# Optimization experiments

Measured on AMD Instinct MI355X. Metric: run time of the kernel, lower is better.

Reference implementation:

```python
import jax, jax.numpy as jnp
import numpy as np

EMB_DIM = 256
N_EMBED = 1024
BETA = 0.25


def setup_inputs() -> dict:
    key = jax.random.key(0)
    k1, k2 = jax.random.split(key)
    encoderout = jax.random.normal(k1, (32, EMB_DIM, 32, 32), dtype=jnp.float32)
    # embedding.weight.data.normal_(mean=0, std=1/n_embed)
    codebook = jax.random.normal(k2, (N_EMBED, EMB_DIM), dtype=jnp.float32) * (1.0 / N_EMBED)
    return {"encoderout": encoderout, "codebook": codebook}


def reference(encoderout, codebook):
    # NCHW -> NHWC
    x = jnp.transpose(encoderout, (0, 2, 3, 1))  # [B,H,W,D]
    flat = x.reshape(-1, EMB_DIM)                # [N,D]
    d2 = (jnp.sum(flat * flat, axis=1, keepdims=True)
          + jnp.sum(codebook * codebook, axis=1)[None, :]
          - 2.0 * flat @ codebook.T)             # [N,K]
    idx = jnp.argmin(d2, axis=1)                 # [N]
    quant = codebook[idx].reshape(x.shape)       # [B,H,W,D]
    codebook_loss = jnp.mean((quant - jax.lax.stop_gradient(x)) ** 2)
    commitment_loss = jnp.mean((x - jax.lax.stop_gradient(quant)) ** 2)
    loss = codebook_loss + BETA * commitment_loss
    # FAITHFUL to source bug: straight-through output is overwritten by the
    # input permuted back to NCHW, so out == encoderout.
    out = jnp.transpose(x, (0, 3, 1, 2))
    return (out, loss, codebook_loss, commitment_loss)
```

## Files before the change

### kernel.cpp

```cpp
#include <hip/hip_runtime.h>
#include <stdint.h>


#define EMB 256
#define ELEMS 8388608

typedef __bf16 bf16x8 __attribute__((ext_vector_type(8)));
typedef float  f32x4  __attribute__((ext_vector_type(4)));

union Frag { uint4 u4; bf16x8 v; };

__device__ __forceinline__ unsigned short f2bf(float f) {
    unsigned u = __float_as_uint(f);
    u += 0x7FFFu + ((u >> 16) & 1u);
    return (unsigned short)(u >> 16);
}

__global__ __launch_bounds__(256) void vq_prep(const float* __restrict__ cb,
                                               uint2* __restrict__ cbswz,
                                               float* __restrict__ esq) {
    const int tid  = threadIdx.x;
    const int w    = tid >> 6;
    const int lane = tid & 63;
    const int n    = blockIdx.x * 4 + w;

    const float4* row = (const float4*)(cb + n * EMB);
    float4 v = row[lane];

    float s = v.x * v.x + v.y * v.y + v.z * v.z + v.w * v.w;
    #pragma unroll
    for (int m = 1; m <= 32; m <<= 1) s += __shfl_xor(s, m);
    if (lane == 0) esq[n] = s;

    unsigned lo = (unsigned)f2bf(v.x) | ((unsigned)f2bf(v.y) << 16);
    unsigned hi = (unsigned)f2bf(v.z) | ((unsigned)f2bf(v.w) << 16);
    int kc = lane >> 1;
    int h  = lane & 1;
    cbswz[n * 64 + ((kc ^ (n & 7)) << 1) + h] = make_uint2(lo, hi);
}

__global__ __launch_bounds__(512, 2) void vq_main(const float* __restrict__ enc,
                                                  const uint4* __restrict__ cbswz,
                                                  const float* __restrict__ esq,
                                                  float* __restrict__ out,
                                                  float* __restrict__ accum) {
    __shared__ uint4 As[2048];
    __shared__ uint4 Bs[2048];
    __shared__ float dmin[4][64];
    __shared__ float partsA[8];

    const int tid  = threadIdx.x;
    const int w    = tid >> 6;
    const int lane = tid & 63;
    const int q    = lane >> 4;
    const int c    = lane & 15;
    const int wm   = w >> 2;
    const int wn   = w & 3;

    const int b   = blockIdx.x >> 4;
    const int hw0 = (blockIdx.x & 15) << 6;
    const float* encB = enc + (size_t)b * 262144 + hw0;
    float*       outB = out + (size_t)b * 262144 + hw0;

    const int q4 = tid & 15;
    const int kg = tid >> 4;
    union { float4 f4; float f[4]; } v[8];
    #pragma unroll
    for (int j = 0; j < 8; ++j)
        v[j].f4 = *(const float4*)(encB + (size_t)(kg * 8 + j) * 1024 + q4 * 4);

    float sx = 0.f;
    #pragma unroll
    for (int j = 0; j < 8; ++j) {
        *(float4*)(outB + (size_t)(kg * 8 + j) * 1024 + q4 * 4) = v[j].f4;
        sx = fmaf(v[j].f[0], v[j].f[0], sx);
        sx = fmaf(v[j].f[1], v[j].f[1], sx);
        sx = fmaf(v[j].f[2], v[j].f[2], sx);
        sx = fmaf(v[j].f[3], v[j].f[3], sx);
    }
    #pragma unroll
    for (int i = 0; i < 4; ++i) {
        unsigned short us[8];
        #pragma unroll
        for (int j = 0; j < 8; ++j) us[j] = f2bf(v[j].f[i]);
        uint4 pk;
        pk.x = (unsigned)us[0] | ((unsigned)us[1] << 16);
        pk.y = (unsigned)us[2] | ((unsigned)us[3] << 16);
        pk.z = (unsigned)us[4] | ((unsigned)us[5] << 16);
        pk.w = (unsigned)us[6] | ((unsigned)us[7] << 16);
        const int r = q4 * 4 + i;
        As[r * 32 + (kg ^ (r & 7))] = pk;
    }
    #pragma unroll
    for (int m = 1; m <= 32; m <<= 1) sx += __shfl_xor(sx, m);
    if (lane == 0) partsA[w] = sx;
    __syncthreads();

    bf16x8 afr[2][8];
    #pragma unroll
    for (int mi = 0; mi < 2; ++mi) {
        const int r = wm * 32 + mi * 16 + c;
        #pragma unroll
        for (int ks = 0; ks < 8; ++ks) {
            Frag fa; fa.u4 = As[r * 32 + ((ks * 4 + q) ^ (r & 7))];
            afr[mi][ks] = fa.v;
        }
    }

    float rmin[2][4];
    #pragma unroll
    for (int mi = 0; mi < 2; ++mi)
        #pragma unroll
        for (int r2 = 0; r2 < 4; ++r2) rmin[mi][r2] = 1e30f;

    const char* cbbase = (const char*)cbswz;
    const int nl = wn * 16 + c;

    for (int nc = 0; nc < 16; ++nc) {
        __syncthreads();
        #pragma unroll
        for (int i = 0; i < 4; ++i) {
            const int o = (i * 8 + w) * 1024;
            __builtin_amdgcn_global_load_lds(
                (const __attribute__((address_space(1))) unsigned int*)
                    (cbbase + nc * 32768 + o + lane * 16),
                (__attribute__((address_space(3))) unsigned int*)((char*)Bs + o),
                16, 0, 0);
        }
        __syncthreads();

        f32x4 acc0 = (f32x4){0.f, 0.f, 0.f, 0.f};
        f32x4 acc1 = (f32x4){0.f, 0.f, 0.f, 0.f};
        #pragma unroll
        for (int ks = 0; ks < 8; ++ks) {
            Frag fb; fb.u4 = Bs[nl * 32 + ((ks * 4 + q) ^ (nl & 7))];
            acc0 = __builtin_amdgcn_mfma_f32_16x16x32_bf16(afr[0][ks], fb.v, acc0, 0, 0, 0);
            acc1 = __builtin_amdgcn_mfma_f32_16x16x32_bf16(afr[1][ks], fb.v, acc1, 0, 0, 0);
        }
        const float eq = esq[nc * 64 + nl];
        #pragma unroll
        for (int r2 = 0; r2 < 4; ++r2) {
            rmin[0][r2] = fminf(rmin[0][r2], fmaf(-2.f, acc0[r2], eq));
            rmin[1][r2] = fminf(rmin[1][r2], fmaf(-2.f, acc1[r2], eq));
        }
    }

    #pragma unroll
    for (int mi = 0; mi < 2; ++mi)
        #pragma unroll
        for (int r2 = 0; r2 < 4; ++r2) {
            float x = rmin[mi][r2];
            x = fminf(x, __shfl_xor(x, 1));
            x = fminf(x, __shfl_xor(x, 2));
            x = fminf(x, __shfl_xor(x, 4));
            x = fminf(x, __shfl_xor(x, 8));
            rmin[mi][r2] = x;
        }
    if (c == 0) {
        #pragma unroll
        for (int mi = 0; mi < 2; ++mi)
            #pragma unroll
            for (int r2 = 0; r2 < 4; ++r2)
                dmin[wn][wm * 32 + mi * 16 + q * 4 + r2] = rmin[mi][r2];
    }
    __syncthreads();

    if (tid < 64) {
        float vr = fminf(fminf(dmin[0][tid], dmin[1][tid]),
                         fminf(dmin[2][tid], dmin[3][tid]));
        #pragma unroll
        for (int m = 1; m <= 32; m <<= 1) vr += __shfl_xor(vr, m);
        if (tid == 0) {
            float s = vr;
            #pragma unroll
            for (int w2 = 0; w2 < 8; ++w2) s += partsA[w2];
            atomicAdd(accum, s);
        }
    }
}

__global__ void vq_finish(const float* __restrict__ accum, float* __restrict__ out) {
    if (threadIdx.x == 0) {
        float cbl = accum[0] * (1.0f / (float)ELEMS);
        out[ELEMS + 0] = 1.25f * cbl;
        out[ELEMS + 1] = cbl;
        out[ELEMS + 2] = cbl;
    }
}

extern "C" void kernel_launch(void* const* d_in, const int* in_sizes, int n_in,
                              void* d_out, int out_size, void* d_ws, size_t ws_size,
                              hipStream_t stream) {
    const float* enc = (const float*)d_in[0];
    const float* cb  = (const float*)d_in[1];
    float* out = (float*)d_out;

    float* accum = (float*)d_ws;
    float* esq   = (float*)((char*)d_ws + 256);
    uint2* cbswz = (uint2*)((char*)d_ws + 8192);

    hipMemsetAsync(d_ws, 0, 4, stream);
    vq_prep<<<dim3(256), dim3(256), 0, stream>>>(cb, cbswz, esq);
    vq_main<<<dim3(512), dim3(512), 0, stream>>>(enc, (const uint4*)cbswz, esq,
                                                 out, accum);
    vq_finish<<<dim3(1), dim3(64), 0, stream>>>(accum, out);
}
```

Baseline: 112.5 us.

## Double-buffer codebook tiles, double rows per block, fold finish into main kernel

Each block now handles 128 spatial rows instead of 64, so every codebook tile loaded into LDS is reused across twice as many rows, and the grid drops to 256 blocks. Codebook chunks are double-buffered: the A staging buffer is reused as the second B buffer, so the next chunk's global-to-LDS load overlaps with the MFMA work on the current one. The memset and the finish kernel are removed. The accumulator is zeroed in the prep kernel, and the last block to finish, detected through an atomic counter, writes the losses. This cuts two launches and some syncs, but it uses more registers for the A fragments and leaves fewer blocks to fill the CUs.

```diff
diff --git a/kernel.cpp b/kernel.cpp
--- a/kernel.cpp
+++ b/kernel.cpp
@@ -4,6 +4,7 @@
 
 #define EMB 256
 #define ELEMS 8388608
+#define NBLK 256
 
 typedef __bf16 bf16x8 __attribute__((ext_vector_type(8)));
 typedef float  f32x4  __attribute__((ext_vector_type(4)));
@@ -18,7 +19,11 @@
 
 __global__ __launch_bounds__(256) void vq_prep(const float* __restrict__ cb,
                                                uint2* __restrict__ cbswz,
-                                               float* __restrict__ esq) {
+                                               float* __restrict__ esq,
+                                               float* __restrict__ accum,
+                                               unsigned* __restrict__ done) {
+    if (blockIdx.x == 0 && threadIdx.x == 0) { accum[0] = 0.f; done[0] = 0u; }
+
     const int tid  = threadIdx.x;
     const int w    = tid >> 6;
     const int lane = tid & 63;
@@ -39,15 +44,53 @@
     cbswz[n * 64 + ((kc ^ (n & 7)) << 1) + h] = make_uint2(lo, hi);
 }
 
+
+#define STAGE(nc_, dst_) do {                                                  \
+    const char* _src = cbbase + (size_t)(nc_) * 32768;                         \
+    _Pragma("unroll")                                                          \
+    for (int _i = 0; _i < 4; ++_i) {                                           \
+        const int _o = (_i * 8 + w) * 1024;         \
+        __builtin_amdgcn_global_load_lds(                                      \
+            (const __attribute__((address_space(1))) unsigned int*)            \
+                (_src + _o + lane * 16),                                       \
+            (__attribute__((address_space(3))) unsigned int*)                  \
+                ((char*)(dst_) + _o),                                          \
+            16, 0, 0);                                                         \
+    } } while (0)
+
+#define CHUNK(nc_, buf_) do {                                                  \
+    f32x4 _a0 = (f32x4){0.f,0.f,0.f,0.f};                                      \
+    f32x4 _a1 = (f32x4){0.f,0.f,0.f,0.f};                                      \
+    f32x4 _a2 = (f32x4){0.f,0.f,0.f,0.f};                                      \
+    f32x4 _a3 = (f32x4){0.f,0.f,0.f,0.f};                                      \
+    _Pragma("unroll")                                                          \
+    for (int _ks = 0; _ks < 8; ++_ks) {                                        \
+        Frag _fb; _fb.u4 = (buf_)[nl * 32 + ((_ks * 4 + q) ^ (nl & 7))];       \
+        _a0 = __builtin_amdgcn_mfma_f32_16x16x32_bf16(afr[0][_ks], _fb.v, _a0, 0, 0, 0); \
+        _a1 = __builtin_amdgcn_mfma_f32_16x16x32_bf16(afr[1][_ks], _fb.v, _a1, 0, 0, 0); \
+        _a2 = __builtin_amdgcn_mfma_f32_16x16x32_bf16(afr[2][_ks], _fb.v, _a2, 0, 0, 0); \
+        _a3 = __builtin_amdgcn_mfma_f32_16x16x32_bf16(afr[3][_ks], _fb.v, _a3, 0, 0, 0); \
+    }                                                                          \
+    const float _eq = esq[(nc_) * 64 + nl];                                    \
+    _Pragma("unroll")                                                          \
+    for (int _r2 = 0; _r2 < 4; ++_r2) {                                        \
+        rmin[0][_r2] = fminf(rmin[0][_r2], fmaf(-2.f, _a0[_r2], _eq));         \
+        rmin[1][_r2] = fminf(rmin[1][_r2], fmaf(-2.f, _a1[_r2], _eq));         \
+        rmin[2][_r2] = fminf(rmin[2][_r2], fmaf(-2.f, _a2[_r2], _eq));         \
+        rmin[3][_r2] = fminf(rmin[3][_r2], fmaf(-2.f, _a3[_r2], _eq));         \
+    } } while (0)
+
 __global__ __launch_bounds__(512, 2) void vq_main(const float* __restrict__ enc,
                                                   const uint4* __restrict__ cbswz,
                                                   const float* __restrict__ esq,
                                                   float* __restrict__ out,
-                                                  float* __restrict__ accum) {
-    __shared__ uint4 As[2048];
+                                                  float* __restrict__ accum,
+                                                  unsigned* __restrict__ done) {
+    __shared__ uint4 As[4096];
     __shared__ uint4 Bs[2048];
-    __shared__ float dmin[4][64];
+    __shared__ float dmin[4][128];
     __shared__ float partsA[8];
+    __shared__ float partsB[2];
 
     const int tid  = threadIdx.x;
     const int w    = tid >> 6;
@@ -57,49 +100,54 @@
     const int wm   = w >> 2;
     const int wn   = w & 3;
 
-    const int b   = blockIdx.x >> 4;
-    const int hw0 = (blockIdx.x & 15) << 6;
+    const int b   = blockIdx.x >> 3;
+    const int hw0 = (blockIdx.x & 7) << 7;
     const float* encB = enc + (size_t)b * 262144 + hw0;
     float*       outB = out + (size_t)b * 262144 + hw0;
+    const char* cbbase = (const char*)cbswz;
+
+    STAGE(0, Bs);
 
     const int q4 = tid & 15;
     const int kg = tid >> 4;
-    union { float4 f4; float f[4]; } v[8];
-    #pragma unroll
-    for (int j = 0; j < 8; ++j)
-        v[j].f4 = *(const float4*)(encB + (size_t)(kg * 8 + j) * 1024 + q4 * 4);
-
     float sx = 0.f;
     #pragma unroll
-    for (int j = 0; j < 8; ++j) {
-        *(float4*)(outB + (size_t)(kg * 8 + j) * 1024 + q4 * 4) = v[j].f4;
-        sx = fmaf(v[j].f[0], v[j].f[0], sx);
-        sx = fmaf(v[j].f[1], v[j].f[1], sx);
-        sx = fmaf(v[j].f[2], v[j].f[2], sx);
-        sx = fmaf(v[j].f[3], v[j].f[3], sx);
-    }
-    #pragma unroll
-    for (int i = 0; i < 4; ++i) {
-        unsigned short us[8];
-        #pragma unroll
-        for (int j = 0; j < 8; ++j) us[j] = f2bf(v[j].f[i]);
-        uint4 pk;
-        pk.x = (unsigned)us[0] | ((unsigned)us[1] << 16);
-        pk.y = (unsigned)us[2] | ((unsigned)us[3] << 16);
-        pk.z = (unsigned)us[4] | ((unsigned)us[5] << 16);
-        pk.w = (unsigned)us[6] | ((unsigned)us[7] << 16);
-        const int r = q4 * 4 + i;
-        As[r * 32 + (kg ^ (r & 7))] = pk;
+    for (int h2 = 0; h2 < 2; ++h2) {
+        union { float4 f4; float f[4]; } v[8];
+        #pragma unroll
+        for (int j = 0; j < 8; ++j)
+            v[j].f4 = *(const float4*)(encB + (size_t)(kg * 8 + j) * 1024 + h2 * 64 + q4 * 4);
+        #pragma unroll
+        for (int j = 0; j < 8; ++j) {
+            *(float4*)(outB + (size_t)(kg * 8 + j) * 1024 + h2 * 64 + q4 * 4) = v[j].f4;
+            sx = fmaf(v[j].f[0], v[j].f[0], sx);
+            sx = fmaf(v[j].f[1], v[j].f[1], sx);
+            sx = fmaf(v[j].f[2], v[j].f[2], sx);
+            sx = fmaf(v[j].f[3], v[j].f[3], sx);
+        }
+        #pragma unroll
+        for (int i = 0; i < 4; ++i) {
+            unsigned short us[8];
+            #pragma unroll
+            for (int j = 0; j < 8; ++j) us[j] = f2bf(v[j].f[i]);
+            uint4 pk;
+            pk.x = (unsigned)us[0] | ((unsigned)us[1] << 16);
+            pk.y = (unsigned)us[2] | ((unsigned)us[3] << 16);
+            pk.z = (unsigned)us[4] | ((unsigned)us[5] << 16);
+            pk.w = (unsigned)us[6] | ((unsigned)us[7] << 16);
+            const int r = h2 * 64 + q4 * 4 + i;
+            As[r * 32 + (kg ^ (r & 7))] = pk;
+        }
     }
     #pragma unroll
     for (int m = 1; m <= 32; m <<= 1) sx += __shfl_xor(sx, m);
     if (lane == 0) partsA[w] = sx;
     __syncthreads();
 
-    bf16x8 afr[2][8];
-    #pragma unroll
-    for (int mi = 0; mi < 2; ++mi) {
-        const int r = wm * 32 + mi * 16 + c;
+    bf16x8 afr[4][8];
+    #pragma unroll
+    for (int mi = 0; mi < 4; ++mi) {
+        const int r = wm * 64 + mi * 16 + c;
         #pragma unroll
         for (int ks = 0; ks < 8; ++ks) {
             Frag fa; fa.u4 = As[r * 32 + ((ks * 4 + q) ^ (r & 7))];
@@ -107,46 +155,27 @@
         }
     }
 
-    float rmin[2][4];
-    #pragma unroll
-    for (int mi = 0; mi < 2; ++mi)
+    float rmin[4][4];
+    #pragma unroll
+    for (int mi = 0; mi < 4; ++mi)
         #pragma unroll
         for (int r2 = 0; r2 < 4; ++r2) rmin[mi][r2] = 1e30f;
 
-    const char* cbbase = (const char*)cbswz;
     const int nl = wn * 16 + c;
 
-    for (int nc = 0; nc < 16; ++nc) {
+    __syncthreads();
+
+    for (int i = 0; i < 8; ++i) {
+        if (i) __syncthreads();
+        STAGE(2 * i + 1, As);
+        CHUNK(2 * i, Bs);
         __syncthreads();
-        #pragma unroll
-        for (int i = 0; i < 4; ++i) {
-            const int o = (i * 8 + w) * 1024;
-            __builtin_amdgcn_global_load_lds(
-                (const __attribute__((address_space(1))) unsigned int*)
-                    (cbbase + nc * 32768 + o + lane * 16),
-                (__attribute__((address_space(3))) unsigned int*)((char*)Bs + o),
-                16, 0, 0);
-        }
-        __syncthreads();
-
-        f32x4 acc0 = (f32x4){0.f, 0.f, 0.f, 0.f};
-        f32x4 acc1 = (f32x4){0.f, 0.f, 0.f, 0.f};
-        #pragma unroll
-        for (int ks = 0; ks < 8; ++ks) {
-            Frag fb; fb.u4 = Bs[nl * 32 + ((ks * 4 + q) ^ (nl & 7))];
-            acc0 = __builtin_amdgcn_mfma_f32_16x16x32_bf16(afr[0][ks], fb.v, acc0, 0, 0, 0);
-            acc1 = __builtin_amdgcn_mfma_f32_16x16x32_bf16(afr[1][ks], fb.v, acc1, 0, 0, 0);
-        }
-        const float eq = esq[nc * 64 + nl];
-        #pragma unroll
-        for (int r2 = 0; r2 < 4; ++r2) {
-            rmin[0][r2] = fminf(rmin[0][r2], fmaf(-2.f, acc0[r2], eq));
-            rmin[1][r2] = fminf(rmin[1][r2], fmaf(-2.f, acc1[r2], eq));
-        }
-    }
-
-    #pragma unroll
-    for (int mi = 0; mi < 2; ++mi)
+        if (i < 7) STAGE(2 * i + 2, Bs);
+        CHUNK(2 * i + 1, (const uint4*)As);
+    }
+
+    #pragma unroll
+    for (int mi = 0; mi < 4; ++mi)
         #pragma unroll
         for (int r2 = 0; r2 < 4; ++r2) {
             float x = rmin[mi][r2];
@@ -158,33 +187,36 @@
         }
     if (c == 0) {
         #pragma unroll
-        for (int mi = 0; mi < 2; ++mi)
+        for (int mi = 0; mi < 4; ++mi)
             #pragma unroll
             for (int r2 = 0; r2 < 4; ++r2)
-                dmin[wn][wm * 32 + mi * 16 + q * 4 + r2] = rmin[mi][r2];
-    }
-    __syncthreads();
-
-    if (tid < 64) {
+                dmin[wn][wm * 64 + mi * 16 + q * 4 + r2] = rmin[mi][r2];
+    }
+    __syncthreads();
+
+    if (tid < 128) {
         float vr = fminf(fminf(dmin[0][tid], dmin[1][tid]),
                          fminf(dmin[2][tid], dmin[3][tid]));
         #pragma unroll
         for (int m = 1; m <= 32; m <<= 1) vr += __shfl_xor(vr, m);
-        if (tid == 0) {
-            float s = vr;
-            #pragma unroll
-            for (int w2 = 0; w2 < 8; ++w2) s += partsA[w2];
-            atomicAdd(accum, s);
-        }
-    }
-}
-
-__global__ void vq_finish(const float* __restrict__ accum, float* __restrict__ out) {
-    if (threadIdx.x == 0) {
-        float cbl = accum[0] * (1.0f / (float)ELEMS);
-        out[ELEMS + 0] = 1.25f * cbl;
-        out[ELEMS + 1] = cbl;
-        out[ELEMS + 2] = cbl;
+        if ((tid & 63) == 0) partsB[tid >> 6] = vr;
+    }
+    __syncthreads();
+
+    if (tid == 0) {
+        float s = partsB[0] + partsB[1];
+        #pragma unroll
+        for (int w2 = 0; w2 < 8; ++w2) s += partsA[w2];
+        atomicAdd(accum, s);
+        __threadfence();
+        unsigned prev = atomicAdd(done, 1u);
+        if (prev == NBLK - 1) {
+            float tot = atomicAdd(accum, 0.0f);
+            float cbl = tot * (1.0f / (float)ELEMS);
+            out[ELEMS + 0] = 1.25f * cbl;
+            out[ELEMS + 1] = cbl;
+            out[ELEMS + 2] = cbl;
+        }
     }
 }
 
@@ -195,13 +227,12 @@
     const float* cb  = (const float*)d_in[1];
     float* out = (float*)d_out;
 
-    float* accum = (float*)d_ws;
-    float* esq   = (float*)((char*)d_ws + 256);
-    uint2* cbswz = (uint2*)((char*)d_ws + 8192);
-
-    hipMemsetAsync(d_ws, 0, 4, stream);
-    vq_prep<<<dim3(256), dim3(256), 0, stream>>>(cb, cbswz, esq);
-    vq_main<<<dim3(512), dim3(512), 0, stream>>>(enc, (const uint4*)cbswz, esq,
-                                                 out, accum);
-    vq_finish<<<dim3(1), dim3(64), 0, stream>>>(accum, out);
-}
+    float*    accum = (float*)d_ws;
+    unsigned* done  = (unsigned*)((char*)d_ws + 64);
+    float*    esq   = (float*)((char*)d_ws + 256);
+    uint2*    cbswz = (uint2*)((char*)d_ws + 8192);
+
+    vq_prep<<<dim3(256), dim3(256), 0, stream>>>(cb, cbswz, esq, accum, done);
+    vq_main<<<dim3(NBLK), dim3(512), 0, stream>>>(enc, (const uint4*)cbswz, esq,
+                                                  out, accum, done);
+}
```

Result: faster. 109.1 us (-3.0%).
